# Performance work log

Hardware: AMD Instinct MI355X
Metric: run time of the kernel (lower is better)

## Reference

```python
import jax, jax.numpy as jnp
import numpy as np
from jax import lax

B, C, H, L = 4, 64, 8, 2048  # batch, per-head channels, heads, sequence length


def setup_inputs() -> dict:
    key = jax.random.key(0)
    ks = jax.random.split(key, 15)

    def p(k, shape, s=0.05):
        return jax.random.normal(k, shape, jnp.float32) * s

    inp = {"x": jax.random.normal(ks[0], (B, C, L), jnp.float32)}
    for i, nm in enumerate(["q", "k", "v"]):
        inp[f"{nm}_dw"] = p(ks[1 + 4 * i], (C, 1, 3))       # depthwise conv weight, groups=C, k=3
        inp[f"{nm}_db"] = p(ks[2 + 4 * i], (C,))
        inp[f"{nm}_pw"] = p(ks[3 + 4 * i], (H * C, C))      # pointwise 1x1 conv weight
        inp[f"{nm}_pb"] = p(ks[4 + 4 * i], (H * C,))
    inp["u_w"] = p(ks[13], (C, H * C))                      # unify_heads 1x1 conv weight
    inp["u_b"] = p(ks[14], (C,))
    return inp


def dsconv(x, dw, db, pw, pb):
    # Depth-separable conv1d: depthwise (k=3, pad=1, groups=C) then pointwise 1x1.
    c = x.shape[1]
    y = lax.conv_general_dilated(x, dw, window_strides=(1,), padding=[(1, 1)],
                                 dimension_numbers=("NCH", "OIH", "NCH"),
                                 feature_group_count=c)
    y = y + db[None, :, None]
    return jnp.einsum("bcl,oc->bol", y, pw) + pb[None, :, None]


def reference(x, q_dw, q_db, q_pw, q_pb, k_dw, k_db, k_pw, k_pb,
              v_dw, v_db, v_pw, v_pb, u_w, u_b):
    b, c, l = x.shape
    h = H
    scale = c ** (-0.25)
    q = dsconv(x, q_dw, q_db, q_pw, q_pb).reshape(b, h, c, l) * scale
    k = dsconv(x, k_dw, k_db, k_pw, k_pb).reshape(b, h, c, l) * scale
    v = dsconv(x, v_dw, v_db, v_pw, v_pb).reshape(b, h, c, l)
    # dot[b,h,i,j] = sum_c k[b,h,c,i] * q[b,h,c,j]  (i = key pos, j = query pos)
    dot = jnp.einsum("bhci,bhcj->bhij", k, q)
    att = jax.nn.softmax(dot, axis=2)  # normalize over key positions (torch dim=1 of [bh,l,l])
    out = jnp.einsum("bhci,bhij->bhcj", v, att).reshape(b, h * c, l)
    return jnp.einsum("bkl,ck->bcl", out, u_w) + u_b[None, :, None]
```

## Files before the change

### kernel.cpp

```cpp
#include <hip/hip_runtime.h>
#include <hip/hip_bf16.h>
#include <stdint.h>
#include <string.h>

typedef unsigned short u16;
typedef unsigned int u32;
typedef __bf16 bf16x8 __attribute__((ext_vector_type(8)));
typedef float f32x4 __attribute__((ext_vector_type(4)));
typedef unsigned int u32x2v __attribute__((ext_vector_type(2)));

#define NB 4
#define NC 64
#define NH 8
#define NL 2048
#define HC 512

#define XT_OFF  ((size_t)0)
#define WM_OFF  ((size_t)1 << 20)
#define PBM_OFF ((size_t)2 << 20)
#define V_OFF   ((size_t)4 << 20)
#define QT_OFF  ((size_t)12 << 20)
#define KT_OFF  ((size_t)20 << 20)

#define LP 68

#if __has_builtin(__builtin_amdgcn_exp2f)
#define EXP2F __builtin_amdgcn_exp2f
#else
#define EXP2F exp2f
#endif

static __device__ __forceinline__ u16 f2bfu(float f) {
  union { float f; unsigned int i; } x; x.f = f;
  unsigned int i = x.i;
  return (u16)((i + 0x7fffu + ((i >> 16) & 1u)) >> 16);
}
static __device__ __forceinline__ u32 pk2(float a, float b) {
  float2 f; f.x = a; f.y = b;
  __hip_bfloat162 h = __float22bfloat162_rn(f);
  u32 w; __builtin_memcpy(&w, &h, 4); return w;
}
static __device__ __forceinline__ bf16x8 ld_bf8(const u16* p) {
  bf16x8 v; __builtin_memcpy(&v, p, 16); return v;
}
static __device__ __forceinline__ bf16x8 frag_from4(u32 a, u32 b, u32 c, u32 d) {
  u32 t[4] = {a, b, c, d};
  bf16x8 v; __builtin_memcpy(&v, t, 16); return v;
}
static __device__ __forceinline__ void st_frag(u16* p, u32 a, u32 b, u32 c, u32 d) {
  u32 t[4] = {a, b, c, d};
  __builtin_memcpy(p, t, 16);
}

#define XCHG(X_, Y_, Fa_, Fb_)                                              \
  {                                                                         \
    u32x2v a_ = __builtin_amdgcn_permlane32_swap((X_), (Y_), false, false); \
    u32x2v b_ = __builtin_amdgcn_permlane16_swap(a_.x, a_.y, false, false); \
    Fa_ = b_.x; Fb_ = b_.y;                                                 \
  }

__global__ __launch_bounds__(256) void prep_all(
    const float* __restrict__ x,
    const float* __restrict__ qdw, const float* __restrict__ qdb,
    const float* __restrict__ qpw, const float* __restrict__ qpb,
    const float* __restrict__ kdw, const float* __restrict__ kdb,
    const float* __restrict__ kpw, const float* __restrict__ kpb,
    const float* __restrict__ vdw, const float* __restrict__ vdb,
    const float* __restrict__ vpw, const float* __restrict__ vpb,
    const float* __restrict__ ub,
    u16* __restrict__ Wm, float* __restrict__ pbm,
    u16* __restrict__ xT, float* __restrict__ out)
{
  __shared__ __align__(16) u16 T[64 * LP];
  int bx = blockIdx.x;
  int tid = threadIdx.x;

  if (bx < 512) {
    int i4 = bx * 256 + tid;
    int c = (i4 >> 9) & 63;
    float f = ub[c];
    float4 v = {f, f, f, f};
    ((float4*)out)[i4] = v;
    return;
  }
  if (bx < 902) {
    int idx = (bx - 512) * 256 + tid;
    if (idx < 98304) {
      int tns = idx >> 15, r = idx & 32767, o = r >> 6, c = r & 63;
      const float* dw = (tns == 0) ? qdw : (tns == 1) ? kdw : vdw;
      const float* pw = (tns == 0) ? qpw : (tns == 1) ? kpw : vpw;
      float s = (tns == 0) ? 0.35355339059327373f * 1.4426950408889634f
              : (tns == 1) ? 0.35355339059327373f : 1.0f;
      float w = pw[o * 64 + c] * s;
#pragma unroll
      for (int d = 0; d < 3; ++d)
        Wm[((size_t)(tns * 3 + d) * 512 + o) * 64 + c] = f2bfu(w * dw[c * 3 + d]);
    } else {
      int i = idx - 98304;
      int tns = i >> 9, o = i & 511;
      const float* db = (tns == 0) ? qdb : (tns == 1) ? kdb : vdb;
      const float* pw = (tns == 0) ? qpw : (tns == 1) ? kpw : vpw;
      const float* pb = (tns == 0) ? qpb : (tns == 1) ? kpb : vpb;
      float s = (tns == 0) ? 0.35355339059327373f * 1.4426950408889634f
              : (tns == 1) ? 0.35355339059327373f : 1.0f;
      float bias = pb[o];
      for (int c = 0; c < 64; ++c) bias += pw[o * 64 + c] * db[c];
      pbm[i] = bias * s;
    }
    return;
  }
  {
    int b2 = bx - 902;
    int lt = b2 & 31, b = b2 >> 5;
    {
      int c = tid & 63, ls = (tid >> 6) * 16;
      const float4* g = (const float4*)(x + ((size_t)b * NC + c) * NL + lt * 64 + ls);
      u16 tmp[16];
#pragma unroll
      for (int j4 = 0; j4 < 4; ++j4) {
        float4 f = g[j4];
        tmp[j4*4+0] = f2bfu(f.x); tmp[j4*4+1] = f2bfu(f.y);
        tmp[j4*4+2] = f2bfu(f.z); tmp[j4*4+3] = f2bfu(f.w);
      }
#pragma unroll
      for (int j = 0; j < 16; ++j) T[(ls + j) * LP + c] = tmp[j];
    }
    __syncthreads();
    {
      int r = tid >> 2, cs = (tid & 3) * 16;
      uint4 a = *(const uint4*)&T[r * LP + cs];
      uint4 b3 = *(const uint4*)&T[r * LP + cs + 8];
      u16* o = xT + ((size_t)b * NL + lt * 64 + r) * 64 + cs;
      *(uint4*)o = a;
      *(uint4*)(o + 8) = b3;
    }
  }
}

__global__ __launch_bounds__(256) void qkv_gemm(
    const u16* __restrict__ xT, const u16* __restrict__ Wm,
    const float* __restrict__ pbm,
    u16* __restrict__ v, u16* __restrict__ qT, u16* __restrict__ kT)
{
  __shared__ __align__(16) u16 WS[3][64 * LP];
  __shared__ __align__(16) u16 XS[130 * LP];

  int bx = blockIdx.x;
  int lg  = bx & 15;
  int och = (bx >> 4) & 7;
  int tmp = bx >> 7;
  int tns = tmp % 3;
  int b   = tmp / 3;

  int tid = threadIdx.x;
  int wave = tid >> 6, lane = tid & 63, quad = lane >> 4, l16 = lane & 15;
  const u16* xg = xT + (size_t)b * NL * 64;
  int L0 = lg * 128;
  uint4 Z = {0, 0, 0, 0};

  {
    const u16* wg = Wm + ((size_t)(tns * 3) * 512 + och * 64) * 64;
#pragma unroll
    for (int it = 0; it < 6; ++it) {
      int s = tid + it * 256;
      int d = s >> 9, r = s & 511;
      int o = r >> 3, c4 = r & 7;
      uint4 w = *(const uint4*)(wg + ((size_t)d * 512 + o) * 64 + c4 * 8);
      *(uint4*)&WS[d][o * LP + c4 * 8] = w;
    }
  }
  {
    int xr = tid >> 3, xc = (tid & 7) * 8;
#pragma unroll
    for (int j = 0; j < 4; ++j) {
      int r = xr + 32 * j;
      int g = L0 - 1 + r;
      uint4 w = ((unsigned)g < NL) ? *(const uint4*)(xg + (size_t)g * 64 + xc) : Z;
      *(uint4*)&XS[r * LP + xc] = w;
    }
    if (tid < 16) {
      int r = 128 + (tid >> 3);
      int g = L0 - 1 + r;
      uint4 w = ((unsigned)g < NL) ? *(const uint4*)(xg + (size_t)g * 64 + xc) : Z;
      *(uint4*)&XS[r * LP + xc] = w;
    }
  }
  __syncthreads();

  f32x4 acc[8] = {{0,0,0,0},{0,0,0,0},{0,0,0,0},{0,0,0,0},
                  {0,0,0,0},{0,0,0,0},{0,0,0,0},{0,0,0,0}};

  if (tns != 2) {
    float4 bq4[4];
    const float* pbt = pbm + tns * 512 + och * 64;
#pragma unroll
    for (int nt = 0; nt < 4; ++nt)
      bq4[nt] = *(const float4*)(pbt + nt * 16 + quad * 4);

#pragma unroll
    for (int d = 0; d < 3; ++d)
#pragma unroll
      for (int kh = 0; kh < 2; ++kh) {
        bf16x8 wf[4], xf[2];
#pragma unroll
        for (int nt = 0; nt < 4; ++nt)
          wf[nt] = ld_bf8(&WS[d][(nt * 16 + l16) * LP + kh * 32 + quad * 8]);
#pragma unroll
        for (int lt = 0; lt < 2; ++lt)
          xf[lt] = ld_bf8(&XS[(wave * 32 + lt * 16 + l16 + d) * LP + kh * 32 + quad * 8]);
#pragma unroll
        for (int nt = 0; nt < 4; ++nt)
#pragma unroll
          for (int lt = 0; lt < 2; ++lt)
            acc[nt * 2 + lt] = __builtin_amdgcn_mfma_f32_16x16x32_bf16(
                wf[nt], xf[lt], acc[nt * 2 + lt], 0, 0, 0);
      }

    u16* dst = (tns == 0) ? qT : kT;
#pragma unroll
    for (int lt = 0; lt < 2; ++lt) {
      u32 w01[4], w23[4];
#pragma unroll
      for (int nt = 0; nt < 4; ++nt) {
        w01[nt] = pk2(acc[nt * 2 + lt][0] + bq4[nt].x, acc[nt * 2 + lt][1] + bq4[nt].y);
        w23[nt] = pk2(acc[nt * 2 + lt][2] + bq4[nt].z, acc[nt * 2 + lt][3] + bq4[nt].w);
      }
      int l = L0 + wave * 32 + lt * 16 + l16;
      u16* qp = dst + ((size_t)(b * 8 + och) * NL + l) * 64;
#pragma unroll
      for (int kh = 0; kh < 2; ++kh) {
        u32 F0, F1, F2, F3;
        XCHG(w01[2 * kh], w01[2 * kh + 1], F0, F2);
        XCHG(w23[2 * kh], w23[2 * kh + 1], F1, F3);
        st_frag(qp + kh * 32 + quad * 8, F0, F1, F2, F3);
      }
    }
  } else {
    float bv4[4];
#pragma unroll
    for (int ot = 0; ot < 4; ++ot)
      bv4[ot] = pbm[tns * 512 + och * 64 + ot * 16 + l16];

#pragma unroll
    for (int d = 0; d < 3; ++d)
#pragma unroll
      for (int kh = 0; kh < 2; ++kh) {
        bf16x8 wf[4], xf[2];
#pragma unroll
        for (int ot = 0; ot < 4; ++ot)
          wf[ot] = ld_bf8(&WS[d][(ot * 16 + l16) * LP + kh * 32 + quad * 8]);
#pragma unroll
        for (int lt = 0; lt < 2; ++lt)
          xf[lt] = ld_bf8(&XS[(wave * 32 + lt * 16 + l16 + d) * LP + kh * 32 + quad * 8]);
#pragma unroll
        for (int lt = 0; lt < 2; ++lt)
#pragma unroll
          for (int ot = 0; ot < 4; ++ot)
            acc[lt * 4 + ot] = __builtin_amdgcn_mfma_f32_16x16x32_bf16(
                xf[lt], wf[ot], acc[lt * 4 + ot], 0, 0, 0);
      }

#pragma unroll
    for (int ot = 0; ot < 4; ++ot) {
      u32 a01[2], a23[2];
#pragma unroll
      for (int lt = 0; lt < 2; ++lt) {
        a01[lt] = pk2(acc[lt * 4 + ot][0] + bv4[ot], acc[lt * 4 + ot][1] + bv4[ot]);
        a23[lt] = pk2(acc[lt * 4 + ot][2] + bv4[ot], acc[lt * 4 + ot][3] + bv4[ot]);
      }
      u16* vp = v + ((size_t)(b * HC + och * 64 + ot * 16 + l16)) * NL + L0 + wave * 32;
      u32 F0, F1, F2, F3;
      XCHG(a01[0], a01[1], F0, F2);
      XCHG(a23[0], a23[1], F1, F3);
      st_frag(vp + quad * 8, F0, F1, F2, F3);
    }
  }
}

__global__ __launch_bounds__(512, 4) void attn_kernel(
    const u16* __restrict__ qT, const u16* __restrict__ kT,
    const u16* __restrict__ vg, const float* __restrict__ uw,
    float* __restrict__ outg)
{
  __shared__ __align__(16) u16 Kt[2][64 * LP];
  __shared__ __align__(16) u16 Vt[2][64 * LP];
  __shared__ __align__(16) u16 UW[64 * LP];

  int bx = blockIdx.x;
  int qt = bx & 15, bh = bx >> 4;
  int b = bh >> 3, h = bh & 7;
  int tid = threadIdx.x;
  int wave = tid >> 6, lane = tid & 63, quad = lane >> 4, l16 = lane & 15;

  const u16* Qh = qT + (size_t)bh * NL * 64;
  const u16* Kh = kT + (size_t)bh * NL * 64;
  const u16* Vh = vg + ((size_t)(b * HC + h * NC)) * NL;
  int q0 = qt * 128;

  int sr = tid >> 3, ss = (tid & 7) * 8;
  int vc = tid >> 3, vk = (tid & 7) * 8;

  {
    int c = tid >> 3, g = (tid & 7) * 8;
    const float4* s = (const float4*)(uw + (size_t)c * HC + h * 64 + g);
    float4 w0 = s[0], w1 = s[1];
    u16* d = &UW[c * LP + g];
    d[0] = f2bfu(w0.x); d[1] = f2bfu(w0.y); d[2] = f2bfu(w0.z); d[3] = f2bfu(w0.w);
    d[4] = f2bfu(w1.x); d[5] = f2bfu(w1.y); d[6] = f2bfu(w1.z); d[7] = f2bfu(w1.w);
  }

  uint4 ka, va;
  {
    ka = *(const uint4*)(Kh + (size_t)sr * 64 + ss);
    va = *(const uint4*)(Vh + (size_t)vc * NL + vk);
    *(uint4*)&Kt[0][sr * LP + ss] = ka;
    *(uint4*)&Vt[0][vc * LP + vk] = va;
    ka = *(const uint4*)(Kh + (size_t)(64 + sr) * 64 + ss);
    va = *(const uint4*)(Vh + (size_t)vc * NL + 64 + vk);
  }

  bf16x8 bq[2];
#pragma unroll
  for (int kh = 0; kh < 2; ++kh)
    bq[kh] = ld_bf8(Qh + (size_t)(q0 + wave * 16 + l16) * 64 + kh * 32 + quad * 8);

  bf16x8 ones = frag_from4(0x3F803F80u, 0x3F803F80u, 0x3F803F80u, 0x3F803F80u);

  __syncthreads();

  f32x4 o[4];
#pragma unroll
  for (int ct = 0; ct < 4; ++ct) o[ct] = (f32x4){0, 0, 0, 0};
  f32x4 lacc = {0, 0, 0, 0};

  for (int i = 0; i < 32; ++i) {
    int cur = i & 1;
    bf16x8 ak[4][2], av[4][2];
#pragma unroll
    for (int j = 0; j < 4; ++j)
#pragma unroll
      for (int kh = 0; kh < 2; ++kh) {
        ak[j][kh] = ld_bf8(&Kt[cur][(j * 16 + l16) * LP + kh * 32 + quad * 8]);
        av[j][kh] = ld_bf8(&Vt[cur][(j * 16 + l16) * LP + kh * 32 + quad * 8]);
      }

    f32x4 s[4];
#pragma unroll
    for (int ktl = 0; ktl < 4; ++ktl) {
      f32x4 z = {0, 0, 0, 0};
      z = __builtin_amdgcn_mfma_f32_16x16x32_bf16(ak[ktl][0], bq[0], z, 0, 0, 0);
      z = __builtin_amdgcn_mfma_f32_16x16x32_bf16(ak[ktl][1], bq[1], z, 0, 0, 0);
      s[ktl] = z;
    }
    u32 w01[4], w23[4];
#pragma unroll
    for (int ktl = 0; ktl < 4; ++ktl) {
      float p0 = EXP2F(s[ktl][0]);
      float p1 = EXP2F(s[ktl][1]);
      float p2 = EXP2F(s[ktl][2]);
      float p3 = EXP2F(s[ktl][3]);
      w01[ktl] = pk2(p0, p1);
      w23[ktl] = pk2(p2, p3);
    }
#pragma unroll
    for (int kh = 0; kh < 2; ++kh) {
      u32 F0, F1, F2, F3;
      XCHG(w01[2 * kh], w01[2 * kh + 1], F0, F2);
      XCHG(w23[2 * kh], w23[2 * kh + 1], F1, F3);
      bf16x8 bp = frag_from4(F0, F1, F2, F3);
      lacc = __builtin_amdgcn_mfma_f32_16x16x32_bf16(ones, bp, lacc, 0, 0, 0);
#pragma unroll
      for (int ct = 0; ct < 4; ++ct)
        o[ct] = __builtin_amdgcn_mfma_f32_16x16x32_bf16(av[ct][kh], bp, o[ct], 0, 0, 0);
    }

    if (i < 31) {
      int nxt = cur ^ 1;
      *(uint4*)&Kt[nxt][sr * LP + ss] = ka;
      *(uint4*)&Vt[nxt][vc * LP + vk] = va;
      if (i < 30) {
        int kt2 = (i + 2) * 64;
        ka = *(const uint4*)(Kh + (size_t)(kt2 + sr) * 64 + ss);
        va = *(const uint4*)(Vh + (size_t)vc * NL + kt2 + vk);
      }
    }
    __syncthreads();
  }

  float* ob = outg + ((size_t)b * NC) * NL;
  {
    float rinv = 1.0f / lacc[0];

    u32 w01[4], w23[4];
#pragma unroll
    for (int ct = 0; ct < 4; ++ct) {
      w01[ct] = pk2(o[ct][0] * rinv, o[ct][1] * rinv);
      w23[ct] = pk2(o[ct][2] * rinv, o[ct][3] * rinv);
    }
    bf16x8 ot[2];
#pragma unroll
    for (int kh = 0; kh < 2; ++kh) {
      u32 F0, F1, F2, F3;
      XCHG(w01[2 * kh], w01[2 * kh + 1], F0, F2);
      XCHG(w23[2 * kh], w23[2 * kh + 1], F1, F3);
      ot[kh] = frag_from4(F0, F1, F2, F3);
    }

    int qcol = q0 + wave * 16 + l16;
#pragma unroll
    for (int mt = 0; mt < 4; ++mt) {
      f32x4 acc = {0, 0, 0, 0};
#pragma unroll
      for (int kh = 0; kh < 2; ++kh) {
        bf16x8 a = ld_bf8(&UW[(mt * 16 + l16) * LP + kh * 32 + quad * 8]);
        acc = __builtin_amdgcn_mfma_f32_16x16x32_bf16(a, ot[kh], acc, 0, 0, 0);
      }
#pragma unroll
      for (int rr = 0; rr < 4; ++rr) {
        int c = mt * 16 + quad * 4 + rr;
        atomicAdd(&ob[(size_t)c * NL + qcol], acc[rr]);
      }
    }
  }
}

extern "C" void kernel_launch(void* const* d_in, const int* in_sizes, int n_in,
                              void* d_out, int out_size, void* d_ws, size_t ws_size,
                              hipStream_t stream) {
  (void)in_sizes; (void)n_in; (void)out_size; (void)ws_size;
  const float* x   = (const float*)d_in[0];
  const float* qdw = (const float*)d_in[1];
  const float* qdb = (const float*)d_in[2];
  const float* qpw = (const float*)d_in[3];
  const float* qpb = (const float*)d_in[4];
  const float* kdw = (const float*)d_in[5];
  const float* kdb = (const float*)d_in[6];
  const float* kpw = (const float*)d_in[7];
  const float* kpb = (const float*)d_in[8];
  const float* vdw = (const float*)d_in[9];
  const float* vdb = (const float*)d_in[10];
  const float* vpw = (const float*)d_in[11];
  const float* vpb = (const float*)d_in[12];
  const float* uw  = (const float*)d_in[13];
  const float* ub  = (const float*)d_in[14];

  char* ws = (char*)d_ws;
  u16*   xT  = (u16*)(ws + XT_OFF);
  u16*   Wm  = (u16*)(ws + WM_OFF);
  float* pbm = (float*)(ws + PBM_OFF);
  u16*   v   = (u16*)(ws + V_OFF);
  u16*   qT  = (u16*)(ws + QT_OFF);
  u16*   kT  = (u16*)(ws + KT_OFF);
  float* out = (float*)d_out;

  prep_all<<<1030, 256, 0, stream>>>(
      x, qdw, qdb, qpw, qpb, kdw, kdb, kpw, kpb, vdw, vdb, vpw, vpb,
      ub, Wm, pbm, xT, out);
  qkv_gemm<<<1536, 256, 0, stream>>>(xT, Wm, pbm, v, qT, kT);
  attn_kernel<<<512, 512, 0, stream>>>(qT, kT, v, uw, out);
}
```

Before: 153.3 us.

## Fuse prep, QKV GEMM and attention into one cooperative persistent kernel

```diff
diff --git a/kernel.cpp b/kernel.cpp
--- a/kernel.cpp
+++ b/kernel.cpp
@@ -1,7 +1,10 @@
 #include <hip/hip_runtime.h>
+#include <hip/hip_cooperative_groups.h>
 #include <hip/hip_bf16.h>
 #include <stdint.h>
 #include <string.h>
+
+namespace cg = cooperative_groups;
 
 typedef unsigned short u16;
 typedef unsigned int u32;
@@ -23,6 +26,7 @@
 #define KT_OFF  ((size_t)20 << 20)
 
 #define LP 68
+#define TILE_U16 (64 * LP)
 
 #if __has_builtin(__builtin_amdgcn_exp2f)
 #define EXP2F __builtin_amdgcn_exp2f
@@ -58,6 +62,347 @@
     u32x2v b_ = __builtin_amdgcn_permlane16_swap(a_.x, a_.y, false, false); \
     Fa_ = b_.x; Fb_ = b_.y;                                                 \
   }
+
+__global__ __launch_bounds__(512, 4) void fused_all(
+    const float* __restrict__ x,
+    const float* __restrict__ qdw, const float* __restrict__ qdb,
+    const float* __restrict__ qpw, const float* __restrict__ qpb,
+    const float* __restrict__ kdw, const float* __restrict__ kdb,
+    const float* __restrict__ kpw, const float* __restrict__ kpb,
+    const float* __restrict__ vdw, const float* __restrict__ vdb,
+    const float* __restrict__ vpw, const float* __restrict__ vpb,
+    const float* __restrict__ ub,  const float* __restrict__ uw,
+    u16* __restrict__ Wm, float* __restrict__ pbm, u16* __restrict__ xT,
+    u16* __restrict__ v, u16* __restrict__ qT, u16* __restrict__ kT,
+    float* __restrict__ outg)
+{
+  __shared__ __align__(16) char LB[43792];
+  cg::grid_group grid = cg::this_grid();
+
+  int bx = blockIdx.x;
+  int tid = threadIdx.x;
+  int wave = tid >> 6, lane = tid & 63, quad = lane >> 4, l16 = lane & 15;
+
+  {
+    int idx = bx * 512 + tid;
+    if (idx < 65536) {
+#pragma unroll
+      for (int jj = 0; jj < 2; ++jj) {
+        int i4 = idx * 2 + jj;
+        int c = (i4 >> 9) & 63;
+        float f = ub[c];
+        float4 vv = {f, f, f, f};
+        ((float4*)outg)[i4] = vv;
+      }
+    } else if (idx < 165376) {
+      int widx = idx - 65536;
+      if (widx < 98304) {
+        int tns = widx >> 15, r = widx & 32767, o = r >> 6, c = r & 63;
+        const float* dw = (tns == 0) ? qdw : (tns == 1) ? kdw : vdw;
+        const float* pw = (tns == 0) ? qpw : (tns == 1) ? kpw : vpw;
+        float s = (tns == 0) ? 0.35355339059327373f * 1.4426950408889634f
+                : (tns == 1) ? 0.35355339059327373f : 1.0f;
+        float w = pw[o * 64 + c] * s;
+#pragma unroll
+        for (int d = 0; d < 3; ++d)
+          Wm[((size_t)(tns * 3 + d) * 512 + o) * 64 + c] = f2bfu(w * dw[c * 3 + d]);
+      } else {
+        int i = widx - 98304;
+        int tns = i >> 9, o = i & 511;
+        const float* db = (tns == 0) ? qdb : (tns == 1) ? kdb : vdb;
+        const float* pw = (tns == 0) ? qpw : (tns == 1) ? kpw : vpw;
+        const float* pb = (tns == 0) ? qpb : (tns == 1) ? kpb : vpb;
+        float s = (tns == 0) ? 0.35355339059327373f * 1.4426950408889634f
+                : (tns == 1) ? 0.35355339059327373f : 1.0f;
+        float bias = pb[o];
+        for (int c = 0; c < 64; ++c) bias += pw[o * 64 + c] * db[c];
+        pbm[i] = bias * s;
+      }
+    } else if (idx < 198144) {
+      int t = idx - 165376;
+      int j = t >> 8, tid8 = t & 255, sub = tid >> 8;
+      u16* T = (u16*)LB + sub * TILE_U16;
+      int lt = j & 31, bb = j >> 5;
+      {
+        int c = tid8 & 63, ls = (tid8 >> 6) * 16;
+        const float4* g = (const float4*)(x + ((size_t)bb * NC + c) * NL + lt * 64 + ls);
+        u16 tmp[16];
+#pragma unroll
+        for (int j4 = 0; j4 < 4; ++j4) {
+          float4 f = g[j4];
+          tmp[j4*4+0] = f2bfu(f.x); tmp[j4*4+1] = f2bfu(f.y);
+          tmp[j4*4+2] = f2bfu(f.z); tmp[j4*4+3] = f2bfu(f.w);
+        }
+#pragma unroll
+        for (int jj = 0; jj < 16; ++jj) T[(ls + jj) * LP + c] = tmp[jj];
+      }
+      __syncthreads();
+      {
+        int r = tid8 >> 2, cs = (tid8 & 3) * 16;
+        uint4 a = *(const uint4*)&T[r * LP + cs];
+        uint4 b3 = *(const uint4*)&T[r * LP + cs + 8];
+        u16* o = xT + ((size_t)bb * NL + lt * 64 + r) * 64 + cs;
+        *(uint4*)o = a;
+        *(uint4*)(o + 8) = b3;
+      }
+    }
+  }
+  grid.sync();
+
+  {
+    u16* WS = (u16*)LB;
+    u16* XS = (u16*)(LB + 26112);
+    uint4 Z = {0, 0, 0, 0};
+
+    for (int u = 0; u < 3; ++u) {
+      int g = bx + u * 512;
+      int lg = g & 15, och = (g >> 4) & 7, tmp2 = g >> 7;
+      int tns = tmp2 % 3, b = tmp2 / 3;
+      int L0 = lg * 128;
+      const u16* xg = xT + (size_t)b * NL * 64;
+
+      {
+        const u16* wg = Wm + ((size_t)(tns * 3) * 512 + och * 64) * 64;
+#pragma unroll
+        for (int it = 0; it < 3; ++it) {
+          int s = tid + it * 512;
+          int d = s >> 9, r = s & 511, o = r >> 3, c4 = r & 7;
+          uint4 w = *(const uint4*)(wg + ((size_t)d * 512 + o) * 64 + c4 * 8);
+          *(uint4*)&WS[(size_t)d * TILE_U16 + o * LP + c4 * 8] = w;
+        }
+      }
+      {
+        int xr = tid >> 3, xc = (tid & 7) * 8;
+#pragma unroll
+        for (int jj = 0; jj < 2; ++jj) {
+          int r = xr + 64 * jj;
+          int gl = L0 - 1 + r;
+          uint4 w = ((unsigned)gl < NL) ? *(const uint4*)(xg + (size_t)gl * 64 + xc) : Z;
+          *(uint4*)&XS[r * LP + xc] = w;
+        }
+        if (tid < 16) {
+          int r = 128 + (tid >> 3);
+          int gl = L0 - 1 + r;
+          uint4 w = ((unsigned)gl < NL) ? *(const uint4*)(xg + (size_t)gl * 64 + xc) : Z;
+          *(uint4*)&XS[r * LP + xc] = w;
+        }
+      }
+      __syncthreads();
+
+      if (tns != 2) {
+        f32x4 acc[4] = {{0,0,0,0},{0,0,0,0},{0,0,0,0},{0,0,0,0}};
+#pragma unroll
+        for (int d = 0; d < 3; ++d)
+#pragma unroll
+          for (int kh = 0; kh < 2; ++kh) {
+            bf16x8 xf = ld_bf8(&XS[(wave * 16 + l16 + d) * LP + kh * 32 + quad * 8]);
+#pragma unroll
+            for (int nt = 0; nt < 4; ++nt) {
+              bf16x8 wf = ld_bf8(&WS[(size_t)d * TILE_U16 + (nt * 16 + l16) * LP + kh * 32 + quad * 8]);
+              acc[nt] = __builtin_amdgcn_mfma_f32_16x16x32_bf16(wf, xf, acc[nt], 0, 0, 0);
+            }
+          }
+        float4 bq4[4];
+        const float* pbt = pbm + tns * 512 + och * 64;
+#pragma unroll
+        for (int nt = 0; nt < 4; ++nt)
+          bq4[nt] = *(const float4*)(pbt + nt * 16 + quad * 4);
+        u32 w01[4], w23[4];
+#pragma unroll
+        for (int nt = 0; nt < 4; ++nt) {
+          w01[nt] = pk2(acc[nt][0] + bq4[nt].x, acc[nt][1] + bq4[nt].y);
+          w23[nt] = pk2(acc[nt][2] + bq4[nt].z, acc[nt][3] + bq4[nt].w);
+        }
+        int l = L0 + wave * 16 + l16;
+        u16* dst = (tns == 0) ? qT : kT;
+        u16* qp = dst + ((size_t)(b * 8 + och) * NL + l) * 64;
+#pragma unroll
+        for (int kh = 0; kh < 2; ++kh) {
+          u32 F0, F1, F2, F3;
+          XCHG(w01[2 * kh], w01[2 * kh + 1], F0, F2);
+          XCHG(w23[2 * kh], w23[2 * kh + 1], F1, F3);
+          st_frag(qp + kh * 32 + quad * 8, F0, F1, F2, F3);
+        }
+      } else {
+        int ot4 = wave & 3, lh = wave >> 2;
+        f32x4 acc[4] = {{0,0,0,0},{0,0,0,0},{0,0,0,0},{0,0,0,0}};
+#pragma unroll
+        for (int d = 0; d < 3; ++d)
+#pragma unroll
+          for (int kh = 0; kh < 2; ++kh) {
+            bf16x8 wf = ld_bf8(&WS[(size_t)d * TILE_U16 + (ot4 * 16 + l16) * LP + kh * 32 + quad * 8]);
+#pragma unroll
+            for (int lt = 0; lt < 4; ++lt) {
+              bf16x8 xf = ld_bf8(&XS[(lh * 64 + lt * 16 + l16 + d) * LP + kh * 32 + quad * 8]);
+              acc[lt] = __builtin_amdgcn_mfma_f32_16x16x32_bf16(xf, wf, acc[lt], 0, 0, 0);
+            }
+          }
+        float bvv = pbm[2 * 512 + och * 64 + ot4 * 16 + l16];
+        u32 a01[4], a23[4];
+#pragma unroll
+        for (int lt = 0; lt < 4; ++lt) {
+          a01[lt] = pk2(acc[lt][0] + bvv, acc[lt][1] + bvv);
+          a23[lt] = pk2(acc[lt][2] + bvv, acc[lt][3] + bvv);
+        }
+        u16* vp = v + ((size_t)(b * HC + och * 64 + ot4 * 16 + l16)) * NL + L0 + lh * 64;
+        {
+          u32 F0, F1, F2, F3;
+          XCHG(a01[0], a01[1], F0, F2);
+          XCHG(a23[0], a23[1], F1, F3);
+          st_frag(vp + quad * 8, F0, F1, F2, F3);
+        }
+        {
+          u32 F0, F1, F2, F3;
+          XCHG(a01[2], a01[3], F0, F2);
+          XCHG(a23[2], a23[3], F1, F3);
+          st_frag(vp + 32 + quad * 8, F0, F1, F2, F3);
+        }
+      }
+      if (u < 2) __syncthreads();
+    }
+  }
+  grid.sync();
+
+  {
+    u16* KT0 = (u16*)LB;
+    u16* VT0 = (u16*)(LB + 17408);
+    u16* UW  = (u16*)(LB + 34816);
+
+    int qt = bx & 15, bh = bx >> 4;
+    int b = bh >> 3, h = bh & 7;
+
+    const u16* Qh = qT + (size_t)bh * NL * 64;
+    const u16* Kh = kT + (size_t)bh * NL * 64;
+    const u16* Vh = v + ((size_t)(b * HC + h * NC)) * NL;
+    int q0 = qt * 128;
+
+    int sr = tid >> 3, ss = (tid & 7) * 8;
+    int vc = tid >> 3, vk = (tid & 7) * 8;
+
+    {
+      int c = tid >> 3, gg = (tid & 7) * 8;
+      const float4* s = (const float4*)(uw + (size_t)c * HC + h * 64 + gg);
+      float4 w0 = s[0], w1 = s[1];
+      u16* d = &UW[c * LP + gg];
+      d[0] = f2bfu(w0.x); d[1] = f2bfu(w0.y); d[2] = f2bfu(w0.z); d[3] = f2bfu(w0.w);
+      d[4] = f2bfu(w1.x); d[5] = f2bfu(w1.y); d[6] = f2bfu(w1.z); d[7] = f2bfu(w1.w);
+    }
+
+    uint4 ka, va;
+    {
+      ka = *(const uint4*)(Kh + (size_t)sr * 64 + ss);
+      va = *(const uint4*)(Vh + (size_t)vc * NL + vk);
+      *(uint4*)&KT0[sr * LP + ss] = ka;
+      *(uint4*)&VT0[vc * LP + vk] = va;
+      ka = *(const uint4*)(Kh + (size_t)(64 + sr) * 64 + ss);
+      va = *(const uint4*)(Vh + (size_t)vc * NL + 64 + vk);
+    }
+
+    bf16x8 bq[2];
+#pragma unroll
+    for (int kh = 0; kh < 2; ++kh)
+      bq[kh] = ld_bf8(Qh + (size_t)(q0 + wave * 16 + l16) * 64 + kh * 32 + quad * 8);
+
+    bf16x8 ones = frag_from4(0x3F803F80u, 0x3F803F80u, 0x3F803F80u, 0x3F803F80u);
+
+    __syncthreads();
+
+    f32x4 o[4];
+#pragma unroll
+    for (int ct = 0; ct < 4; ++ct) o[ct] = (f32x4){0, 0, 0, 0};
+    f32x4 lacc = {0, 0, 0, 0};
+
+    for (int i = 0; i < 32; ++i) {
+      int cur = i & 1;
+      u16* Ktc = KT0 + cur * TILE_U16;
+      u16* Vtc = VT0 + cur * TILE_U16;
+      bf16x8 ak[4][2], av[4][2];
+#pragma unroll
+      for (int j = 0; j < 4; ++j)
+#pragma unroll
+        for (int kh = 0; kh < 2; ++kh) {
+          ak[j][kh] = ld_bf8(&Ktc[(j * 16 + l16) * LP + kh * 32 + quad * 8]);
+          av[j][kh] = ld_bf8(&Vtc[(j * 16 + l16) * LP + kh * 32 + quad * 8]);
+        }
+
+      f32x4 s[4];
+#pragma unroll
+      for (int ktl = 0; ktl < 4; ++ktl) {
+        f32x4 z = {0, 0, 0, 0};
+        z = __builtin_amdgcn_mfma_f32_16x16x32_bf16(ak[ktl][0], bq[0], z, 0, 0, 0);
+        z = __builtin_amdgcn_mfma_f32_16x16x32_bf16(ak[ktl][1], bq[1], z, 0, 0, 0);
+        s[ktl] = z;
+      }
+      u32 w01[4], w23[4];
+#pragma unroll
+      for (int ktl = 0; ktl < 4; ++ktl) {
+        float p0 = EXP2F(s[ktl][0]);
+        float p1 = EXP2F(s[ktl][1]);
+        float p2 = EXP2F(s[ktl][2]);
+        float p3 = EXP2F(s[ktl][3]);
+        w01[ktl] = pk2(p0, p1);
+        w23[ktl] = pk2(p2, p3);
+      }
+#pragma unroll
+      for (int kh = 0; kh < 2; ++kh) {
+        u32 F0, F1, F2, F3;
+        XCHG(w01[2 * kh], w01[2 * kh + 1], F0, F2);
+        XCHG(w23[2 * kh], w23[2 * kh + 1], F1, F3);
+        bf16x8 bp = frag_from4(F0, F1, F2, F3);
+        lacc = __builtin_amdgcn_mfma_f32_16x16x32_bf16(ones, bp, lacc, 0, 0, 0);
+#pragma unroll
+        for (int ct = 0; ct < 4; ++ct)
+          o[ct] = __builtin_amdgcn_mfma_f32_16x16x32_bf16(av[ct][kh], bp, o[ct], 0, 0, 0);
+      }
+
+      if (i < 31) {
+        int nxt = cur ^ 1;
+        *(uint4*)&KT0[nxt * TILE_U16 + sr * LP + ss] = ka;
+        *(uint4*)&VT0[nxt * TILE_U16 + vc * LP + vk] = va;
+        if (i < 30) {
+          int kt2 = (i + 2) * 64;
+          ka = *(const uint4*)(Kh + (size_t)(kt2 + sr) * 64 + ss);
+          va = *(const uint4*)(Vh + (size_t)vc * NL + kt2 + vk);
+        }
+      }
+      __syncthreads();
+    }
+
+    float* ob = outg + ((size_t)b * NC) * NL;
+    {
+      float rinv = 1.0f / lacc[0];
+      u32 w01[4], w23[4];
+#pragma unroll
+      for (int ct = 0; ct < 4; ++ct) {
+        w01[ct] = pk2(o[ct][0] * rinv, o[ct][1] * rinv);
+        w23[ct] = pk2(o[ct][2] * rinv, o[ct][3] * rinv);
+      }
+      bf16x8 ot[2];
+#pragma unroll
+      for (int kh = 0; kh < 2; ++kh) {
+        u32 F0, F1, F2, F3;
+        XCHG(w01[2 * kh], w01[2 * kh + 1], F0, F2);
+        XCHG(w23[2 * kh], w23[2 * kh + 1], F1, F3);
+        ot[kh] = frag_from4(F0, F1, F2, F3);
+      }
+      int qcol = q0 + wave * 16 + l16;
+#pragma unroll
+      for (int mt = 0; mt < 4; ++mt) {
+        f32x4 acc = {0, 0, 0, 0};
+#pragma unroll
+        for (int kh = 0; kh < 2; ++kh) {
+          bf16x8 a = ld_bf8(&UW[(mt * 16 + l16) * LP + kh * 32 + quad * 8]);
+          acc = __builtin_amdgcn_mfma_f32_16x16x32_bf16(a, ot[kh], acc, 0, 0, 0);
+        }
+#pragma unroll
+        for (int rr = 0; rr < 4; ++rr) {
+          int c = mt * 16 + quad * 4 + rr;
+          atomicAdd(&ob[(size_t)c * NL + qcol], acc[rr]);
+        }
+      }
+    }
+  }
+}
 
 __global__ __launch_bounds__(256) void prep_all(
     const float* __restrict__ x,
@@ -390,7 +735,6 @@
   float* ob = outg + ((size_t)b * NC) * NL;
   {
     float rinv = 1.0f / lacc[0];
-
     u32 w01[4], w23[4];
 #pragma unroll
     for (int ct = 0; ct < 4; ++ct) {
@@ -405,7 +749,6 @@
       XCHG(w23[2 * kh], w23[2 * kh + 1], F1, F3);
       ot[kh] = frag_from4(F0, F1, F2, F3);
     }
-
     int qcol = q0 + wave * 16 + l16;
 #pragma unroll
     for (int mt = 0; mt < 4; ++mt) {
@@ -453,9 +796,22 @@
   u16*   kT  = (u16*)(ws + KT_OFF);
   float* out = (float*)d_out;
 
-  prep_all<<<1030, 256, 0, stream>>>(
-      x, qdw, qdb, qpw, qpb, kdw, kdb, kpw, kpb, vdw, vdb, vpw, vpb,
-      ub, Wm, pbm, xT, out);
-  qkv_gemm<<<1536, 256, 0, stream>>>(xT, Wm, pbm, v, qT, kT);
-  attn_kernel<<<512, 512, 0, stream>>>(qT, kT, v, uw, out);
-}
+  void* args[] = {
+      (void*)&x,  (void*)&qdw, (void*)&qdb, (void*)&qpw, (void*)&qpb,
+      (void*)&kdw, (void*)&kdb, (void*)&kpw, (void*)&kpb,
+      (void*)&vdw, (void*)&vdb, (void*)&vpw, (void*)&vpb,
+      (void*)&ub, (void*)&uw,
+      (void*)&Wm, (void*)&pbm, (void*)&xT,
+      (void*)&v, (void*)&qT, (void*)&kT, (void*)&out};
+
+  hipError_t err = hipLaunchCooperativeKernel(
+      (void*)fused_all, dim3(512), dim3(512), args, 0, stream);
+
+  if (err != hipSuccess) {
+    prep_all<<<1030, 256, 0, stream>>>(
+        x, qdw, qdb, qpw, qpb, kdw, kdb, kpw, kpb, vdw, vdb, vpw, vpb,
+        ub, Wm, pbm, xT, out);
+    qkv_gemm<<<1536, 256, 0, stream>>>(xT, Wm, pbm, v, qT, kT);
+    attn_kernel<<<512, 512, 0, stream>>>(qT, kT, v, uw, out);
+  }
+}
```

Result: slower. 318.3 us (+107.6%).
